# Optimization experiments

Hardware: AMD Instinct MI355X
Metric: run time of the kernel (lower is better)

The kernel has to match this reference:

```python
import jax, jax.numpy as jnp
import numpy as np

E, D, H, N = 600000, 128, 256, 50000
LN_EPS = 1e-5


def layer_norm(x, g, b):
    mu = jnp.mean(x, axis=-1, keepdims=True)
    var = jnp.var(x, axis=-1, keepdims=True)
    return (x - mu) * jax.lax.rsqrt(var + LN_EPS) * g + b


def setup_inputs() -> dict:
    key = jax.random.key(0)
    ks = jax.random.split(key, 8)
    edges = jax.random.normal(ks[0], (E, D), dtype=jnp.float32)
    edges_index = jax.random.randint(ks[1], (E,), 0, N, dtype=jnp.int64)
    # params (PyTorch Linear default-ish init scale)
    w1 = jax.random.normal(ks[2], (D, H), dtype=jnp.float32) * (1.0 / np.sqrt(D))
    b1 = jnp.zeros((H,), dtype=jnp.float32)
    w2 = jax.random.normal(ks[3], (H, H), dtype=jnp.float32) * (1.0 / np.sqrt(H))
    b2 = jnp.zeros((H,), dtype=jnp.float32)
    wg = jax.random.normal(ks[4], (H, 1), dtype=jnp.float32) * (1.0 / np.sqrt(H))
    bg = jnp.zeros((1,), dtype=jnp.float32)
    wo = jax.random.normal(ks[5], (H, D), dtype=jnp.float32) * (1.0 / np.sqrt(H))
    bo = jnp.zeros((D,), dtype=jnp.float32)
    return {
        "edges": edges, "edges_index": edges_index, "num_nodes": N,
        "ln1_g": jnp.ones((D,), jnp.float32), "ln1_b": jnp.zeros((D,), jnp.float32),
        "w1": w1, "b1": b1,
        "ln2_g": jnp.ones((H,), jnp.float32), "ln2_b": jnp.zeros((H,), jnp.float32),
        "w2": w2, "b2": b2,
        "wg": wg, "bg": bg,
        "wo": wo, "bo": bo,
    }


def reference(edges, edges_index, num_nodes, ln1_g, ln1_b, w1, b1, ln2_g, ln2_b, w2, b2, wg, bg, wo, bo):
    # edge MLP: LN -> Linear -> ELU -> LN -> Linear
    h = layer_norm(edges, ln1_g, ln1_b)
    h = jax.nn.elu(h @ w1 + b1)
    h = layer_norm(h, ln2_g, ln2_b)
    h = h @ w2 + b2                      # [E, H]
    # gated output projection
    gate = jax.nn.sigmoid(h @ wg + bg)   # [E, 1]
    out = (h @ wo + bo) * gate           # [E, D]
    # scatter_add over destination nodes
    res = jax.ops.segment_sum(out, edges_index, num_segments=num_nodes)  # [N, D]
    return res
```

## Files before the change

kernel.cpp:

```cpp
#include <hip/hip_runtime.h>
#include <hip/hip_bf16.h>

typedef __bf16 bf16x8 __attribute__((ext_vector_type(8)));
typedef float f32x4 __attribute__((ext_vector_type(4)));

#define D 128
#define H 256
#define TM 32
#define THREADS 256
#define LN_EPS 1e-5f
#define NSCAN 50176

__global__ void pack_weights(const float* __restrict__ w1,
                             const float* __restrict__ w2,
                             const float* __restrict__ wo,
                             __bf16* __restrict__ pw) {
    int tid = blockIdx.x * blockDim.x + threadIdx.x;
    const float* W; int K, NN, local;
    if (tid < 32768)       { W = w1; K = 128; NN = 256; local = tid; }
    else if (tid < 98304)  { W = w2; K = 256; NN = 256; local = tid - 32768; }
    else if (tid < 131072) { W = wo; K = 256; NN = 128; local = tid - 98304; }
    else return;
    int b = local >> 9, within = local & 511;
    int l = within >> 3, i = within & 7;
    int nbk = K >> 5;
    int n0 = (b / nbk) << 4, k0 = (b % nbk) << 5;
    int k = k0 + ((l >> 4) << 3) + i;
    int n = n0 + (l & 15);
    pw[tid] = (__bf16)W[k * NN + n];
}

__global__ void zero_out_kernel(float4* __restrict__ out, int n4) {
    int i = blockIdx.x * blockDim.x + threadIdx.x;
    if (i < n4) out[i] = float4{0.f, 0.f, 0.f, 0.f};
}

__global__ void csr_zero_counts(int* __restrict__ counts) {
    int i = blockIdx.x * blockDim.x + threadIdx.x;
    if (i < NSCAN) counts[i] = 0;
}

__global__ void csr_hist(const int* __restrict__ eidx, int* __restrict__ counts,
                         int* __restrict__ pos, int E) {
    int e = blockIdx.x * blockDim.x + threadIdx.x;
    if (e < E) pos[e] = atomicAdd(&counts[eidx[e]], 1);
}

__global__ void csr_scan1(const int* __restrict__ counts, int* __restrict__ offs,
                          int* __restrict__ bsum) {
    __shared__ int wsum[4];
    int tid = threadIdx.x, blk = blockIdx.x;
    int base = blk * 1024 + tid * 4;
    int c0 = counts[base], c1 = counts[base+1], c2 = counts[base+2], c3 = counts[base+3];
    int tot = c0 + c1 + c2 + c3;
    int lane = tid & 63, wv = tid >> 6;
    int inc = tot;
    #pragma unroll
    for (int d = 1; d < 64; d <<= 1) {
        int v = __shfl_up(inc, d);
        if (lane >= d) inc += v;
    }
    if (lane == 63) wsum[wv] = inc;
    __syncthreads();
    int wbase = 0;
    for (int w = 0; w < wv; ++w) wbase += wsum[w];
    int excl = wbase + inc - tot;
    offs[base]   = excl;
    offs[base+1] = excl + c0;
    offs[base+2] = excl + c0 + c1;
    offs[base+3] = excl + c0 + c1 + c2;
    if (tid == 255) bsum[blk] = wbase + inc;
}

__global__ void csr_scan2(int* __restrict__ bsum) {
    int l = threadIdx.x;
    int v = (l < 49) ? bsum[l] : 0;
    int inc = v;
    #pragma unroll
    for (int d = 1; d < 64; d <<= 1) {
        int u = __shfl_up(inc, d);
        if (l >= d) inc += u;
    }
    if (l < 49) bsum[l] = inc - v;
}

__global__ void csr_scan3(int* __restrict__ offs, const int* __restrict__ bsum) {
    int i = blockIdx.x * blockDim.x + threadIdx.x;
    if (i < NSCAN) offs[i] += bsum[i >> 10];
}

__global__ void csr_place(const int* __restrict__ eidx, const int* __restrict__ offs,
                          const int* __restrict__ pos, int* __restrict__ order, int E) {
    int e = blockIdx.x * blockDim.x + threadIdx.x;
    if (e < E) order[offs[eidx[e]] + pos[e]] = e;
}

__global__ __launch_bounds__(256) void gather_kernel(
    const float* __restrict__ eout, const int* __restrict__ offs,
    const int* __restrict__ order, float* __restrict__ out, int N) {
    int wave = threadIdx.x >> 6, lane = threadIdx.x & 63;
    int n = blockIdx.x * 4 + wave;
    if (n >= N) return;
    int beg = offs[n];
    int end = offs[n + 1];
    float ax = 0.f, ay = 0.f;
    float bx = 0.f, by = 0.f;
    int j = beg;
    for (; j + 2 <= end; j += 2) {
        int e1 = order[j], e2 = order[j + 1];
        const float2 v1 = *reinterpret_cast<const float2*>(eout + (size_t)e1 * D + lane * 2);
        const float2 v2 = *reinterpret_cast<const float2*>(eout + (size_t)e2 * D + lane * 2);
        ax += v1.x; ay += v1.y;
        bx += v2.x; by += v2.y;
    }
    if (j < end) {
        int e = order[j];
        const float2 v = *reinterpret_cast<const float2*>(eout + (size_t)e * D + lane * 2);
        ax += v.x; ay += v.y;
    }
    *reinterpret_cast<float2*>(out + (size_t)n * D + lane * 2) = float2{ax + bx, ay + by};
}

__global__ __launch_bounds__(THREADS, 3) void fused_edge_kernel(
    const float* __restrict__ edges, const int* __restrict__ eidx,
    const float* __restrict__ ln1_g, const float* __restrict__ ln1_b,
    const float* __restrict__ b1,
    const float* __restrict__ ln2_g, const float* __restrict__ ln2_b,
    const float* __restrict__ b2,
    const float* __restrict__ wg, const float* __restrict__ bg,
    const float* __restrict__ bo,
    const __bf16* __restrict__ pw,
    float* __restrict__ out, float* __restrict__ eout, int use_eout, int E)
{
    __shared__ __bf16 sH[TM * H];
    __shared__ float sRedS[4][TM];
    __shared__ float sRedQ[4][TM];
    __shared__ float sMu[TM], sRs[TM], sGate[TM];
    __shared__ int   sIdx[TM];
    __bf16* sA = sH;

    const __bf16* pw1 = pw;
    const __bf16* pw2 = pw + 32768;
    const __bf16* pwo = pw + 98304;

    const int t    = threadIdx.x;
    const int lane = t & 63;
    const int wave = t >> 6;
    const int lr   = lane & 15;
    const int lg   = lane >> 4;
    const int e0   = blockIdx.x * TM;

    if (!use_eout && t < TM) sIdx[t] = (e0 + t < E) ? eidx[e0 + t] : 0;

    {
        const int row = t >> 3;
        const int c8  = t & 7;
        const int er  = min(e0 + row, E - 1);
        const float* src = edges + (size_t)er * D + c8 * 16;
        float x[16];
        #pragma unroll
        for (int i = 0; i < 4; ++i) {
            float4 v = reinterpret_cast<const float4*>(src)[i];
            x[i*4+0]=v.x; x[i*4+1]=v.y; x[i*4+2]=v.z; x[i*4+3]=v.w;
        }
        float s = 0.f, sq = 0.f;
        #pragma unroll
        for (int i = 0; i < 16; ++i) { s += x[i]; sq += x[i]*x[i]; }
        s  += __shfl_xor(s, 1);  s  += __shfl_xor(s, 2);  s  += __shfl_xor(s, 4);
        sq += __shfl_xor(sq, 1); sq += __shfl_xor(sq, 2); sq += __shfl_xor(sq, 4);
        const float mu  = s * (1.0f / D);
        const float var = sq * (1.0f / D) - mu * mu;
        const float rs  = rsqrtf(var + LN_EPS);
        const float4* g4 = reinterpret_cast<const float4*>(ln1_g + c8 * 16);
        const float4* b4 = reinterpret_cast<const float4*>(ln1_b + c8 * 16);
        #pragma unroll
        for (int i = 0; i < 2; ++i) {
            float4 ga = g4[2*i], gb = g4[2*i+1];
            float4 ba = b4[2*i], bb = b4[2*i+1];
            float gg[8] = {ga.x, ga.y, ga.z, ga.w, gb.x, gb.y, gb.z, gb.w};
            float bv[8] = {ba.x, ba.y, ba.z, ba.w, bb.x, bb.y, bb.z, bb.w};
            bf16x8 yv;
            #pragma unroll
            for (int j = 0; j < 8; ++j)
                yv[j] = (__bf16)((x[i*8+j] - mu) * rs * gg[j] + bv[j]);
            int idx = (row * D + c8*16 + i*8) ^ ((row & 7) << 3);
            *reinterpret_cast<bf16x8*>(&sA[idx]) = yv;
        }
    }
    __syncthreads();

    f32x4 acc[2][4];
    #pragma unroll
    for (int a = 0; a < 2; ++a)
        #pragma unroll
        for (int b = 0; b < 4; ++b) acc[a][b] = f32x4{0.f,0.f,0.f,0.f};

    #pragma unroll
    for (int ks = 0; ks < 4; ++ks) {
        bf16x8 af[2];
        #pragma unroll
        for (int mt = 0; mt < 2; ++mt) {
            int row = mt*16 + lr;
            int idx = (row * D + ks*32 + lg*8) ^ ((row & 7) << 3);
            af[mt] = *reinterpret_cast<const bf16x8*>(&sA[idx]);
        }
        bf16x8 bv[4];
        #pragma unroll
        for (int nt = 0; nt < 4; ++nt) {
            int blk = (wave*4 + nt) * 4 + ks;
            bv[nt] = *reinterpret_cast<const bf16x8*>(pw1 + blk*512 + lane*8);
        }
        #pragma unroll
        for (int mt = 0; mt < 2; ++mt)
            #pragma unroll
            for (int nt = 0; nt < 4; ++nt)
                acc[mt][nt] = __builtin_amdgcn_mfma_f32_16x16x32_bf16(af[mt], bv[nt], acc[mt][nt], 0, 0, 0);
    }

    float b1v[4];
    #pragma unroll
    for (int nt = 0; nt < 4; ++nt) b1v[nt] = b1[wave*64 + nt*16 + lr];
    {
        float ps[2][4], pq[2][4];
        #pragma unroll
        for (int mt = 0; mt < 2; ++mt)
            #pragma unroll
            for (int r = 0; r < 4; ++r) { ps[mt][r] = 0.f; pq[mt][r] = 0.f; }
        #pragma unroll
        for (int mt = 0; mt < 2; ++mt)
            #pragma unroll
            for (int nt = 0; nt < 4; ++nt)
                #pragma unroll
                for (int r = 0; r < 4; ++r) {
                    float x = acc[mt][nt][r] + b1v[nt];
                    x = x > 0.f ? x : (__expf(x) - 1.0f);
                    acc[mt][nt][r] = x;
                    ps[mt][r] += x;
                    pq[mt][r] += x * x;
                }
        #pragma unroll
        for (int mt = 0; mt < 2; ++mt)
            #pragma unroll
            for (int r = 0; r < 4; ++r) {
                float s = ps[mt][r], q = pq[mt][r];
                s += __shfl_xor(s, 1); s += __shfl_xor(s, 2); s += __shfl_xor(s, 4); s += __shfl_xor(s, 8);
                q += __shfl_xor(q, 1); q += __shfl_xor(q, 2); q += __shfl_xor(q, 4); q += __shfl_xor(q, 8);
                if (lr == 0) {
                    int row = mt*16 + lg*4 + r;
                    sRedS[wave][row] = s;
                    sRedQ[wave][row] = q;
                }
            }
    }
    __syncthreads();
    if (t < TM) {
        float S = sRedS[0][t] + sRedS[1][t] + sRedS[2][t] + sRedS[3][t];
        float Q = sRedQ[0][t] + sRedQ[1][t] + sRedQ[2][t] + sRedQ[3][t];
        float mu  = S * (1.0f / H);
        float var = Q * (1.0f / H) - mu * mu;
        sMu[t] = mu;
        sRs[t] = rsqrtf(var + LN_EPS);
    }
    __syncthreads();

    {
        float g2v[4], bt2[4];
        #pragma unroll
        for (int nt = 0; nt < 4; ++nt) {
            g2v[nt] = ln2_g[wave*64 + nt*16 + lr];
            bt2[nt] = ln2_b[wave*64 + nt*16 + lr];
        }
        #pragma unroll
        for (int mt = 0; mt < 2; ++mt)
            #pragma unroll
            for (int r = 0; r < 4; ++r) {
                int row = mt*16 + lg*4 + r;
                float mu = sMu[row], rs = sRs[row];
                #pragma unroll
                for (int nt = 0; nt < 4; ++nt) {
                    int col = wave*64 + nt*16 + lr;
                    float h = (acc[mt][nt][r] - mu) * rs * g2v[nt] + bt2[nt];
                    int idx = (row * H + col) ^ ((row & 7) << 3);
                    sH[idx] = (__bf16)h;
                }
            }
    }
    __syncthreads();

    #pragma unroll
    for (int a = 0; a < 2; ++a)
        #pragma unroll
        for (int b = 0; b < 4; ++b) acc[a][b] = f32x4{0.f,0.f,0.f,0.f};

    #pragma unroll
    for (int ks = 0; ks < 8; ++ks) {
        bf16x8 af[2];
        #pragma unroll
        for (int mt = 0; mt < 2; ++mt) {
            int row = mt*16 + lr;
            int idx = (row * H + ks*32 + lg*8) ^ ((row & 7) << 3);
            af[mt] = *reinterpret_cast<const bf16x8*>(&sH[idx]);
        }
        bf16x8 bv[4];
        #pragma unroll
        for (int nt = 0; nt < 4; ++nt) {
            int blk = (wave*4 + nt) * 8 + ks;
            bv[nt] = *reinterpret_cast<const bf16x8*>(pw2 + blk*512 + lane*8);
        }
        #pragma unroll
        for (int mt = 0; mt < 2; ++mt)
            #pragma unroll
            for (int nt = 0; nt < 4; ++nt)
                acc[mt][nt] = __builtin_amdgcn_mfma_f32_16x16x32_bf16(af[mt], bv[nt], acc[mt][nt], 0, 0, 0);
    }

    float pg[2][4];
    {
        float b2v[4], wgv[4];
        #pragma unroll
        for (int nt = 0; nt < 4; ++nt) {
            b2v[nt] = b2[wave*64 + nt*16 + lr];
            wgv[nt] = wg[wave*64 + nt*16 + lr];
        }
        #pragma unroll
        for (int mt = 0; mt < 2; ++mt)
            #pragma unroll
            for (int r = 0; r < 4; ++r) pg[mt][r] = 0.f;
        #pragma unroll
        for (int mt = 0; mt < 2; ++mt)
            #pragma unroll
            for (int nt = 0; nt < 4; ++nt)
                #pragma unroll
                for (int r = 0; r < 4; ++r) {
                    float h2 = acc[mt][nt][r] + b2v[nt];
                    acc[mt][nt][r] = h2;
                    pg[mt][r] += h2 * wgv[nt];
                }
        #pragma unroll
        for (int mt = 0; mt < 2; ++mt)
            #pragma unroll
            for (int r = 0; r < 4; ++r) {
                float s = pg[mt][r];
                s += __shfl_xor(s, 1); s += __shfl_xor(s, 2); s += __shfl_xor(s, 4); s += __shfl_xor(s, 8);
                pg[mt][r] = s;
            }
    }
    __syncthreads();
    #pragma unroll
    for (int mt = 0; mt < 2; ++mt)
        #pragma unroll
        for (int r = 0; r < 4; ++r) {
            int row = mt*16 + lg*4 + r;
            #pragma unroll
            for (int nt = 0; nt < 4; ++nt) {
                int col = wave*64 + nt*16 + lr;
                int idx = (row * H + col) ^ ((row & 7) << 3);
                sH[idx] = (__bf16)acc[mt][nt][r];
            }
        }
    if (lr == 0) {
        #pragma unroll
        for (int mt = 0; mt < 2; ++mt)
            #pragma unroll
            for (int r = 0; r < 4; ++r)
                sRedS[wave][mt*16 + lg*4 + r] = pg[mt][r];
    }
    __syncthreads();
    if (t < TM) {
        float z = sRedS[0][t] + sRedS[1][t] + sRedS[2][t] + sRedS[3][t] + bg[0];
        sGate[t] = 1.0f / (1.0f + __expf(-z));
    }
    __syncthreads();

    f32x4 acc3[2][2];
    #pragma unroll
    for (int a = 0; a < 2; ++a)
        #pragma unroll
        for (int b = 0; b < 2; ++b) acc3[a][b] = f32x4{0.f,0.f,0.f,0.f};

    #pragma unroll
    for (int ks = 0; ks < 8; ++ks) {
        bf16x8 af[2];
        #pragma unroll
        for (int mt = 0; mt < 2; ++mt) {
            int row = mt*16 + lr;
            int idx = (row * H + ks*32 + lg*8) ^ ((row & 7) << 3);
            af[mt] = *reinterpret_cast<const bf16x8*>(&sH[idx]);
        }
        bf16x8 bv[2];
        #pragma unroll
        for (int nt = 0; nt < 2; ++nt) {
            int blk = (wave*2 + nt) * 8 + ks;
            bv[nt] = *reinterpret_cast<const bf16x8*>(pwo + blk*512 + lane*8);
        }
        #pragma unroll
        for (int mt = 0; mt < 2; ++mt)
            #pragma unroll
            for (int nt = 0; nt < 2; ++nt)
                acc3[mt][nt] = __builtin_amdgcn_mfma_f32_16x16x32_bf16(af[mt], bv[nt], acc3[mt][nt], 0, 0, 0);
    }

    {
        float bov[2];
        #pragma unroll
        for (int nt = 0; nt < 2; ++nt) bov[nt] = bo[wave*32 + nt*16 + lr];
        if (use_eout) {
            #pragma unroll
            for (int mt = 0; mt < 2; ++mt)
                #pragma unroll
                for (int r = 0; r < 4; ++r) {
                    int row = mt*16 + lg*4 + r;
                    int e = e0 + row;
                    if (e < E) {
                        float gt = sGate[row];
                        float* dst = eout + (size_t)e * D;
                        #pragma unroll
                        for (int nt = 0; nt < 2; ++nt) {
                            int col = wave*32 + nt*16 + lr;
                            dst[col] = (acc3[mt][nt][r] + bov[nt]) * gt;
                        }
                    }
                }
        } else {
            #pragma unroll
            for (int mt = 0; mt < 2; ++mt)
                #pragma unroll
                for (int r = 0; r < 4; ++r) {
                    int row = mt*16 + lg*4 + r;
                    if (e0 + row < E) {
                        int node = sIdx[row];
                        float gt = sGate[row];
                        float* dst = out + (size_t)node * D;
                        #pragma unroll
                        for (int nt = 0; nt < 2; ++nt) {
                            int col = wave*32 + nt*16 + lr;
                            float v = (acc3[mt][nt][r] + bov[nt]) * gt;
                            unsafeAtomicAdd(dst + col, v);
                        }
                    }
                }
        }
    }
}

extern "C" void kernel_launch(void* const* d_in, const int* in_sizes, int n_in,
                              void* d_out, int out_size, void* d_ws, size_t ws_size,
                              hipStream_t stream) {
    const float* edges = (const float*)d_in[0];
    const int*   eidx  = (const int*)d_in[1];
    const float* ln1_g = (const float*)d_in[3];
    const float* ln1_b = (const float*)d_in[4];
    const float* w1    = (const float*)d_in[5];
    const float* b1    = (const float*)d_in[6];
    const float* ln2_g = (const float*)d_in[7];
    const float* ln2_b = (const float*)d_in[8];
    const float* w2    = (const float*)d_in[9];
    const float* b2    = (const float*)d_in[10];
    const float* wg    = (const float*)d_in[11];
    const float* bg    = (const float*)d_in[12];
    const float* wo    = (const float*)d_in[13];
    const float* bo    = (const float*)d_in[14];
    float* out = (float*)d_out;
    const int E = in_sizes[0] / D;
    const int N = out_size / D;

    size_t eout_b  = (size_t)E * D * sizeof(float);
    size_t pw_b    = 131072 * sizeof(__bf16);
    size_t cnt_b   = (size_t)NSCAN * sizeof(int);
    size_t offs_b  = (size_t)(NSCAN + 1) * sizeof(int);
    size_t bsum_b  = 64 * sizeof(int);
    size_t posord_b = (size_t)E * sizeof(int);
    size_t need = eout_b + pw_b + cnt_b + offs_b + bsum_b + 2 * posord_b;

    const int use_csr = (ws_size >= need) ? 1 : 0;

    if (use_csr) {
        float* eout  = (float*)d_ws;
        __bf16* pw   = (__bf16*)((char*)d_ws + eout_b);
        int* counts  = (int*)((char*)pw + pw_b);
        int* offs    = (int*)((char*)counts + cnt_b);
        int* bsum    = (int*)((char*)offs + offs_b);
        int* pos     = (int*)((char*)bsum + bsum_b);
        int* order   = (int*)((char*)pos + posord_b);

        pack_weights<<<512, 256, 0, stream>>>(w1, w2, wo, pw);
        csr_zero_counts<<<NSCAN / 256, 256, 0, stream>>>(counts);
        csr_hist<<<(E + 255) / 256, 256, 0, stream>>>(eidx, counts, pos, E);
        csr_scan1<<<49, 256, 0, stream>>>(counts, offs, bsum);
        csr_scan2<<<1, 64, 0, stream>>>(bsum);
        csr_scan3<<<NSCAN / 256, 256, 0, stream>>>(offs, bsum);
        csr_place<<<(E + 255) / 256, 256, 0, stream>>>(eidx, offs, pos, order, E);
        fused_edge_kernel<<<(E + TM - 1) / TM, THREADS, 0, stream>>>(
            edges, eidx, ln1_g, ln1_b, b1, ln2_g, ln2_b, b2, wg, bg, bo,
            pw, out, eout, 1, E);
        gather_kernel<<<(N + 3) / 4, 256, 0, stream>>>(eout, offs, order, out, N);
    } else {
        __bf16* pw = (__bf16*)d_ws;
        pack_weights<<<512, 256, 0, stream>>>(w1, w2, wo, pw);
        int n4 = out_size / 4;
        zero_out_kernel<<<(n4 + 255) / 256, 256, 0, stream>>>((float4*)d_out, n4);
        fused_edge_kernel<<<(E + TM - 1) / TM, THREADS, 0, stream>>>(
            edges, eidx, ln1_g, ln1_b, b1, ln2_g, ln2_b, b2, wg, bg, bo,
            pw, out, nullptr, 0, E);
    }
}
```

Before: 472.7 us.

## Double edge tile to 64 rows with 8 waves, each computing narrower column slices

```diff
diff --git a/kernel.cpp b/kernel.cpp
--- a/kernel.cpp
+++ b/kernel.cpp
@@ -6,8 +6,8 @@
 
 #define D 128
 #define H 256
-#define TM 32
-#define THREADS 256
+#define TM 64
+#define THREADS 512
 #define LN_EPS 1e-5f
 #define NSCAN 50176
 
@@ -121,7 +121,7 @@
     *reinterpret_cast<float2*>(out + (size_t)n * D + lane * 2) = float2{ax + bx, ay + by};
 }
 
-__global__ __launch_bounds__(THREADS, 3) void fused_edge_kernel(
+__global__ __launch_bounds__(THREADS, 4) void fused_edge_kernel(
     const float* __restrict__ edges, const int* __restrict__ eidx,
     const float* __restrict__ ln1_g, const float* __restrict__ ln1_b,
     const float* __restrict__ b1,
@@ -133,8 +133,8 @@
     float* __restrict__ out, float* __restrict__ eout, int use_eout, int E)
 {
     __shared__ __bf16 sH[TM * H];
-    __shared__ float sRedS[4][TM];
-    __shared__ float sRedQ[4][TM];
+    __shared__ float sRedS[8][TM];
+    __shared__ float sRedQ[8][TM];
     __shared__ float sMu[TM], sRs[TM], sGate[TM];
     __shared__ int   sIdx[TM];
     __bf16* sA = sH;
@@ -189,73 +189,72 @@
     }
     __syncthreads();
 
-    f32x4 acc[2][4];
-    #pragma unroll
-    for (int a = 0; a < 2; ++a)
-        #pragma unroll
-        for (int b = 0; b < 4; ++b) acc[a][b] = f32x4{0.f,0.f,0.f,0.f};
+    f32x4 acc[4][2];
+    #pragma unroll
+    for (int a = 0; a < 4; ++a)
+        #pragma unroll
+        for (int b = 0; b < 2; ++b) acc[a][b] = f32x4{0.f,0.f,0.f,0.f};
 
     #pragma unroll
     for (int ks = 0; ks < 4; ++ks) {
-        bf16x8 af[2];
-        #pragma unroll
-        for (int mt = 0; mt < 2; ++mt) {
+        bf16x8 af[4];
+        #pragma unroll
+        for (int mt = 0; mt < 4; ++mt) {
             int row = mt*16 + lr;
             int idx = (row * D + ks*32 + lg*8) ^ ((row & 7) << 3);
             af[mt] = *reinterpret_cast<const bf16x8*>(&sA[idx]);
         }
-        bf16x8 bv[4];
-        #pragma unroll
-        for (int nt = 0; nt < 4; ++nt) {
-            int blk = (wave*4 + nt) * 4 + ks;
+        bf16x8 bv[2];
+        #pragma unroll
+        for (int nt = 0; nt < 2; ++nt) {
+            int blk = (wave*2 + nt) * 4 + ks;
             bv[nt] = *reinterpret_cast<const bf16x8*>(pw1 + blk*512 + lane*8);
         }
         #pragma unroll
-        for (int mt = 0; mt < 2; ++mt)
-            #pragma unroll
-            for (int nt = 0; nt < 4; ++nt)
+        for (int mt = 0; mt < 4; ++mt)
+            #pragma unroll
+            for (int nt = 0; nt < 2; ++nt)
                 acc[mt][nt] = __builtin_amdgcn_mfma_f32_16x16x32_bf16(af[mt], bv[nt], acc[mt][nt], 0, 0, 0);
     }
 
-    float b1v[4];
-    #pragma unroll
-    for (int nt = 0; nt < 4; ++nt) b1v[nt] = b1[wave*64 + nt*16 + lr];
-    {
-        float ps[2][4], pq[2][4];
-        #pragma unroll
-        for (int mt = 0; mt < 2; ++mt)
-            #pragma unroll
-            for (int r = 0; r < 4; ++r) { ps[mt][r] = 0.f; pq[mt][r] = 0.f; }
-        #pragma unroll
-        for (int mt = 0; mt < 2; ++mt)
-            #pragma unroll
-            for (int nt = 0; nt < 4; ++nt)
-                #pragma unroll
-                for (int r = 0; r < 4; ++r) {
-                    float x = acc[mt][nt][r] + b1v[nt];
-                    x = x > 0.f ? x : (__expf(x) - 1.0f);
-                    acc[mt][nt][r] = x;
-                    ps[mt][r] += x;
-                    pq[mt][r] += x * x;
-                }
-        #pragma unroll
-        for (int mt = 0; mt < 2; ++mt)
+    float b1v[2], g2v[2], bt2v[2];
+    #pragma unroll
+    for (int nt = 0; nt < 2; ++nt) {
+        b1v[nt]  = b1[wave*32 + nt*16 + lr];
+        g2v[nt]  = ln2_g[wave*32 + nt*16 + lr];
+        bt2v[nt] = ln2_b[wave*32 + nt*16 + lr];
+    }
+    #pragma unroll
+    for (int mt = 0; mt < 4; ++mt) {
+        float psr[4] = {0.f,0.f,0.f,0.f};
+        float pqr[4] = {0.f,0.f,0.f,0.f};
+        #pragma unroll
+        for (int nt = 0; nt < 2; ++nt)
             #pragma unroll
             for (int r = 0; r < 4; ++r) {
-                float s = ps[mt][r], q = pq[mt][r];
-                s += __shfl_xor(s, 1); s += __shfl_xor(s, 2); s += __shfl_xor(s, 4); s += __shfl_xor(s, 8);
-                q += __shfl_xor(q, 1); q += __shfl_xor(q, 2); q += __shfl_xor(q, 4); q += __shfl_xor(q, 8);
-                if (lr == 0) {
-                    int row = mt*16 + lg*4 + r;
-                    sRedS[wave][row] = s;
-                    sRedQ[wave][row] = q;
-                }
+                float x = acc[mt][nt][r] + b1v[nt];
+                x = x > 0.f ? x : (__expf(x) - 1.0f);
+                acc[mt][nt][r] = x;
+                psr[r] += x;
+                pqr[r] += x * x;
             }
+        #pragma unroll
+        for (int r = 0; r < 4; ++r) {
+            float s = psr[r], q = pqr[r];
+            s += __shfl_xor(s, 1); s += __shfl_xor(s, 2); s += __shfl_xor(s, 4); s += __shfl_xor(s, 8);
+            q += __shfl_xor(q, 1); q += __shfl_xor(q, 2); q += __shfl_xor(q, 4); q += __shfl_xor(q, 8);
+            if (lr == 0) {
+                int row = mt*16 + lg*4 + r;
+                sRedS[wave][row] = s;
+                sRedQ[wave][row] = q;
+            }
+        }
     }
     __syncthreads();
     if (t < TM) {
-        float S = sRedS[0][t] + sRedS[1][t] + sRedS[2][t] + sRedS[3][t];
-        float Q = sRedQ[0][t] + sRedQ[1][t] + sRedQ[2][t] + sRedQ[3][t];
+        float S = 0.f, Q = 0.f;
+        #pragma unroll
+        for (int w = 0; w < 8; ++w) { S += sRedS[w][t]; Q += sRedQ[w][t]; }
         float mu  = S * (1.0f / H);
         float var = Q * (1.0f / H) - mu * mu;
         sMu[t] = mu;
@@ -263,180 +262,139 @@
     }
     __syncthreads();
 
-    {
-        float g2v[4], bt2[4];
-        #pragma unroll
-        for (int nt = 0; nt < 4; ++nt) {
-            g2v[nt] = ln2_g[wave*64 + nt*16 + lr];
-            bt2[nt] = ln2_b[wave*64 + nt*16 + lr];
-        }
-        #pragma unroll
-        for (int mt = 0; mt < 2; ++mt)
-            #pragma unroll
-            for (int r = 0; r < 4; ++r) {
-                int row = mt*16 + lg*4 + r;
-                float mu = sMu[row], rs = sRs[row];
-                #pragma unroll
-                for (int nt = 0; nt < 4; ++nt) {
-                    int col = wave*64 + nt*16 + lr;
-                    float h = (acc[mt][nt][r] - mu) * rs * g2v[nt] + bt2[nt];
-                    int idx = (row * H + col) ^ ((row & 7) << 3);
-                    sH[idx] = (__bf16)h;
-                }
+    #pragma unroll
+    for (int mt = 0; mt < 4; ++mt)
+        #pragma unroll
+        for (int r = 0; r < 4; ++r) {
+            int row = mt*16 + lg*4 + r;
+            float mu = sMu[row], rs = sRs[row];
+            #pragma unroll
+            for (int nt = 0; nt < 2; ++nt) {
+                int col = wave*32 + nt*16 + lr;
+                float h = (acc[mt][nt][r] - mu) * rs * g2v[nt] + bt2v[nt];
+                int idx = (row * H + col) ^ ((row & 7) << 3);
+                sH[idx] = (__bf16)h;
             }
-    }
-    __syncthreads();
-
-    #pragma unroll
-    for (int a = 0; a < 2; ++a)
-        #pragma unroll
-        for (int b = 0; b < 4; ++b) acc[a][b] = f32x4{0.f,0.f,0.f,0.f};
+        }
+    __syncthreads();
+
+    #pragma unroll
+    for (int a = 0; a < 4; ++a)
+        #pragma unroll
+        for (int b = 0; b < 2; ++b) acc[a][b] = f32x4{0.f,0.f,0.f,0.f};
 
     #pragma unroll
     for (int ks = 0; ks < 8; ++ks) {
-        bf16x8 af[2];
-        #pragma unroll
-        for (int mt = 0; mt < 2; ++mt) {
+        bf16x8 af[4];
+        #pragma unroll
+        for (int mt = 0; mt < 4; ++mt) {
             int row = mt*16 + lr;
             int idx = (row * H + ks*32 + lg*8) ^ ((row & 7) << 3);
             af[mt] = *reinterpret_cast<const bf16x8*>(&sH[idx]);
         }
-        bf16x8 bv[4];
-        #pragma unroll
-        for (int nt = 0; nt < 4; ++nt) {
-            int blk = (wave*4 + nt) * 8 + ks;
+        bf16x8 bv[2];
+        #pragma unroll
+        for (int nt = 0; nt < 2; ++nt) {
+            int blk = (wave*2 + nt) * 8 + ks;
             bv[nt] = *reinterpret_cast<const bf16x8*>(pw2 + blk*512 + lane*8);
         }
         #pragma unroll
-        for (int mt = 0; mt < 2; ++mt)
-            #pragma unroll
-            for (int nt = 0; nt < 4; ++nt)
+        for (int mt = 0; mt < 4; ++mt)
+            #pragma unroll
+            for (int nt = 0; nt < 2; ++nt)
                 acc[mt][nt] = __builtin_amdgcn_mfma_f32_16x16x32_bf16(af[mt], bv[nt], acc[mt][nt], 0, 0, 0);
     }
 
-    float pg[2][4];
     {
-        float b2v[4], wgv[4];
-        #pragma unroll
-        for (int nt = 0; nt < 4; ++nt) {
-            b2v[nt] = b2[wave*64 + nt*16 + lr];
-            wgv[nt] = wg[wave*64 + nt*16 + lr];
-        }
-        #pragma unroll
-        for (int mt = 0; mt < 2; ++mt)
-            #pragma unroll
-            for (int r = 0; r < 4; ++r) pg[mt][r] = 0.f;
-        #pragma unroll
-        for (int mt = 0; mt < 2; ++mt)
-            #pragma unroll
-            for (int nt = 0; nt < 4; ++nt)
+        float b2v[2], wgv[2];
+        #pragma unroll
+        for (int nt = 0; nt < 2; ++nt) {
+            b2v[nt] = b2[wave*32 + nt*16 + lr];
+            wgv[nt] = wg[wave*32 + nt*16 + lr];
+        }
+        #pragma unroll
+        for (int mt = 0; mt < 4; ++mt) {
+            float pgr[4] = {0.f,0.f,0.f,0.f};
+            #pragma unroll
+            for (int nt = 0; nt < 2; ++nt)
                 #pragma unroll
                 for (int r = 0; r < 4; ++r) {
                     float h2 = acc[mt][nt][r] + b2v[nt];
                     acc[mt][nt][r] = h2;
-                    pg[mt][r] += h2 * wgv[nt];
+                    pgr[r] += h2 * wgv[nt];
                 }
-        #pragma unroll
-        for (int mt = 0; mt < 2; ++mt)
             #pragma unroll
             for (int r = 0; r < 4; ++r) {
-                float s = pg[mt][r];
+                float s = pgr[r];
                 s += __shfl_xor(s, 1); s += __shfl_xor(s, 2); s += __shfl_xor(s, 4); s += __shfl_xor(s, 8);
-                pg[mt][r] = s;
+                if (lr == 0) sRedS[wave][mt*16 + lg*4 + r] = s;
             }
-    }
-    __syncthreads();
-    #pragma unroll
-    for (int mt = 0; mt < 2; ++mt)
+        }
+    }
+    __syncthreads();
+    #pragma unroll
+    for (int mt = 0; mt < 4; ++mt)
         #pragma unroll
         for (int r = 0; r < 4; ++r) {
             int row = mt*16 + lg*4 + r;
             #pragma unroll
-            for (int nt = 0; nt < 4; ++nt) {
-                int col = wave*64 + nt*16 + lr;
+            for (int nt = 0; nt < 2; ++nt) {
+                int col = wave*32 + nt*16 + lr;
                 int idx = (row * H + col) ^ ((row & 7) << 3);
                 sH[idx] = (__bf16)acc[mt][nt][r];
             }
         }
-    if (lr == 0) {
-        #pragma unroll
-        for (int mt = 0; mt < 2; ++mt)
-            #pragma unroll
-            for (int r = 0; r < 4; ++r)
-                sRedS[wave][mt*16 + lg*4 + r] = pg[mt][r];
-    }
     __syncthreads();
     if (t < TM) {
-        float z = sRedS[0][t] + sRedS[1][t] + sRedS[2][t] + sRedS[3][t] + bg[0];
+        float z = bg[0];
+        #pragma unroll
+        for (int w = 0; w < 8; ++w) z += sRedS[w][t];
         sGate[t] = 1.0f / (1.0f + __expf(-z));
     }
     __syncthreads();
 
-    f32x4 acc3[2][2];
-    #pragma unroll
-    for (int a = 0; a < 2; ++a)
-        #pragma unroll
-        for (int b = 0; b < 2; ++b) acc3[a][b] = f32x4{0.f,0.f,0.f,0.f};
+    #pragma unroll
+    for (int a = 0; a < 4; ++a) acc[a][0] = f32x4{0.f,0.f,0.f,0.f};
 
     #pragma unroll
     for (int ks = 0; ks < 8; ++ks) {
-        bf16x8 af[2];
-        #pragma unroll
-        for (int mt = 0; mt < 2; ++mt) {
+        bf16x8 af[4];
+        #pragma unroll
+        for (int mt = 0; mt < 4; ++mt) {
             int row = mt*16 + lr;
             int idx = (row * H + ks*32 + lg*8) ^ ((row & 7) << 3);
             af[mt] = *reinterpret_cast<const bf16x8*>(&sH[idx]);
         }
-        bf16x8 bv[2];
-        #pragma unroll
-        for (int nt = 0; nt < 2; ++nt) {
-            int blk = (wave*2 + nt) * 8 + ks;
-            bv[nt] = *reinterpret_cast<const bf16x8*>(pwo + blk*512 + lane*8);
-        }
-        #pragma unroll
-        for (int mt = 0; mt < 2; ++mt)
-            #pragma unroll
-            for (int nt = 0; nt < 2; ++nt)
-                acc3[mt][nt] = __builtin_amdgcn_mfma_f32_16x16x32_bf16(af[mt], bv[nt], acc3[mt][nt], 0, 0, 0);
+        int blk = wave * 8 + ks;
+        bf16x8 bv0 = *reinterpret_cast<const bf16x8*>(pwo + blk*512 + lane*8);
+        #pragma unroll
+        for (int mt = 0; mt < 4; ++mt)
+            acc[mt][0] = __builtin_amdgcn_mfma_f32_16x16x32_bf16(af[mt], bv0, acc[mt][0], 0, 0, 0);
     }
 
     {
-        float bov[2];
-        #pragma unroll
-        for (int nt = 0; nt < 2; ++nt) bov[nt] = bo[wave*32 + nt*16 + lr];
+        const int col = wave*16 + lr;
+        const float bov = bo[col];
         if (use_eout) {
             #pragma unroll
-            for (int mt = 0; mt < 2; ++mt)
+            for (int mt = 0; mt < 4; ++mt)
                 #pragma unroll
                 for (int r = 0; r < 4; ++r) {
                     int row = mt*16 + lg*4 + r;
                     int e = e0 + row;
-                    if (e < E) {
-                        float gt = sGate[row];
-                        float* dst = eout + (size_t)e * D;
-                        #pragma unroll
-                        for (int nt = 0; nt < 2; ++nt) {
-                            int col = wave*32 + nt*16 + lr;
-                            dst[col] = (acc3[mt][nt][r] + bov[nt]) * gt;
-                        }
-                    }
+                    if (e < E)
+                        eout[(size_t)e * D + col] = (acc[mt][0][r] + bov) * sGate[row];
                 }
         } else {
             #pragma unroll
-            for (int mt = 0; mt < 2; ++mt)
+            for (int mt = 0; mt < 4; ++mt)
                 #pragma unroll
                 for (int r = 0; r < 4; ++r) {
                     int row = mt*16 + lg*4 + r;
                     if (e0 + row < E) {
                         int node = sIdx[row];
-                        float gt = sGate[row];
-                        float* dst = out + (size_t)node * D;
-                        #pragma unroll
-                        for (int nt = 0; nt < 2; ++nt) {
-                            int col = wave*32 + nt*16 + lr;
-                            float v = (acc3[mt][nt][r] + bov[nt]) * gt;
-                            unsafeAtomicAdd(dst + col, v);
-                        }
+                        float v = (acc[mt][0][r] + bov) * sGate[row];
+                        unsafeAtomicAdd(out + (size_t)node * D + col, v);
                     }
                 }
         }
```

After: 645.2 us. 36.5% more time.
